# Optimization experiments

Measured on AMD Instinct MI355X. Metric: run time of the kernel, lower is better.

## Reference

```python
import jax, jax.numpy as jnp
import numpy as np

B, T, V, D, L, FFM = 2, 2048, 50257, 1024, 8, 2


def setup_inputs() -> dict:
    key = jax.random.key(0)
    ks = jax.random.split(key, 10)
    s = 0.02
    return {
        "input_ids": jax.random.randint(ks[0], (B, T), 0, V),
        "embed": jax.random.normal(ks[1], (V, D), jnp.float32) * s,
        "norm1_w": jnp.ones((L, D), jnp.float32),
        "norm2_w": jnp.ones((L, D), jnp.float32),
        "a_diag": jax.random.uniform(ks[2], (L, D), jnp.float32, 0.5, 0.99),
        "W_in": jax.random.normal(ks[3], (L, D, D), jnp.float32) * s,
        "b_in": jnp.zeros((L, D), jnp.float32),
        "W_out": jax.random.normal(ks[4], (L, D, D), jnp.float32) * s,
        "ff_w1": jax.random.normal(ks[5], (L, D, FFM * D), jnp.float32) * s,
        "ff_b1": jnp.zeros((L, FFM * D), jnp.float32),
        "ff_w2": jax.random.normal(ks[6], (L, FFM * D, D), jnp.float32) * s,
        "ff_b2": jnp.zeros((L, D), jnp.float32),
        "final_norm_w": jnp.ones((D,), jnp.float32),
        "lm_head_w": jax.random.normal(ks[7], (V, D), jnp.float32) * s,
    }


def rmsnorm(x, w, eps=1e-6):
    return x * jax.lax.rsqrt(jnp.mean(x * x, axis=-1, keepdims=True) + eps) * w


def chaos_core(x, a, Win, bin_, Wout):
    pre = jnp.einsum('btd,de->bte', x, Win) + bin_  # precompute input drive (parallel)

    def step(s, p):
        s = jnp.tanh(a * s + p)
        return s, s

    s0 = jnp.zeros((x.shape[0], x.shape[-1]), x.dtype)
    _, hs = jax.lax.scan(step, s0, jnp.swapaxes(pre, 0, 1))  # (T, B, D)
    hs = jnp.swapaxes(hs, 0, 1)  # (B, T, D)
    return jnp.einsum('btd,de->bte', hs, Wout)


def reference(input_ids, embed, norm1_w, norm2_w, a_diag, W_in, b_in, W_out,
              ff_w1, ff_b1, ff_w2, ff_b2, final_norm_w, lm_head_w):
    x = embed[input_ids]  # (B, T, D)
    for i in range(L):
        # input_norm -> core -> residual
        x = x + chaos_core(rmsnorm(x, norm1_w[i]), a_diag[i], W_in[i], b_in[i], W_out[i])
        # ff_norm -> FeedForward (Linear -> SiLU -> Linear) -> residual
        h = rmsnorm(x, norm2_w[i])
        h = jax.nn.silu(jnp.einsum('btd,df->btf', h, ff_w1[i]) + ff_b1[i])
        x = x + jnp.einsum('btf,fd->btd', h, ff_w2[i]) + ff_b2[i]
    x = rmsnorm(x, final_norm_w)
    return jnp.einsum('btd,vd->btv', x, lm_head_w)  # logits (B, T, V)
```

## Files before the change

### kernel.cpp

```cpp
#include <hip/hip_runtime.h>

typedef unsigned short u16;
typedef __bf16 bf16x8 __attribute__((ext_vector_type(8)));
typedef float f32x4 __attribute__((ext_vector_type(4)));
typedef unsigned short u16x4 __attribute__((ext_vector_type(4)));

__device__ __forceinline__ u16 f2bf(float f) {
  union { float f; unsigned int u; } v; v.f = f;
  return (u16)((v.u + 0x7FFFu + ((v.u >> 16) & 1u)) >> 16);
}

__device__ __forceinline__ void gload16(const void* g, void* l) {
  __builtin_amdgcn_global_load_lds(
      (const __attribute__((address_space(1))) unsigned int*)g,
      (__attribute__((address_space(3))) unsigned int*)l, 16, 0, 0);
}

__global__ __launch_bounds__(256) void prep_all(
    const float* __restrict__ Win, const float* __restrict__ Wout,
    const float* __restrict__ ffw1, const float* __restrict__ ffw2,
    u16* __restrict__ WinT, u16* __restrict__ WoutT,
    u16* __restrict__ f1T, u16* __restrict__ f2T,
    const float* __restrict__ lmw, u16* __restrict__ lmpad,
    const int* __restrict__ ids, const float* __restrict__ embedw,
    float* __restrict__ x) {
  __shared__ float tile[32][33];
  const int bid = blockIdx.x;
  const int tid = threadIdx.x;

  if (bid >= 49152 + 50432) {
    const int row = bid - (49152 + 50432);
    *(float4*)(x + (size_t)row * 1024 + tid * 4) =
        *(const float4*)(embedw + (size_t)ids[row] * 1024 + tid * 4);
    return;
  }
  if (bid >= 49152) {
    const int row = bid - 49152;
    u16x4 o = {0, 0, 0, 0};
    if (row < 50257) {
      float4 v = *(const float4*)(lmw + (size_t)row * 1024 + tid * 4);
      o.x = f2bf(v.x); o.y = f2bf(v.y); o.z = f2bf(v.z); o.w = f2bf(v.w);
    }
    *(u16x4*)(lmpad + (size_t)row * 1024 + tid * 4) = o;
    return;
  }

  const int tk = bid;
  const float* src; u16* dst;
  int R, C, tr, tc;
  if (tk < 8192) {
    const int l = tk >> 10, rem = tk & 1023;
    R = 1024; C = 1024; tr = rem >> 5; tc = rem & 31;
    src = Win + (size_t)l * 1048576; dst = WinT + (size_t)l * 1048576;
  } else if (tk < 16384) {
    const int q = tk - 8192, l = q >> 10, rem = q & 1023;
    R = 1024; C = 1024; tr = rem >> 5; tc = rem & 31;
    src = Wout + (size_t)l * 1048576; dst = WoutT + (size_t)l * 1048576;
  } else if (tk < 32768) {
    const int q = tk - 16384, l = q >> 11, rem = q & 2047;
    R = 1024; C = 2048; tr = rem >> 6; tc = rem & 63;
    src = ffw1 + (size_t)l * 2097152; dst = f1T + (size_t)l * 2097152;
  } else {
    const int q = tk - 32768, l = q >> 11, rem = q & 2047;
    R = 2048; C = 1024; tr = rem >> 5; tc = rem & 31;
    src = ffw2 + (size_t)l * 2097152; dst = f2T + (size_t)l * 2097152;
  }
  const int tx = tid & 31, ty = tid >> 5;
  const int c0 = tc * 32, r0 = tr * 32;
#pragma unroll
  for (int k = 0; k < 32; k += 8)
    tile[ty + k][tx] = src[(size_t)(r0 + ty + k) * C + (c0 + tx)];
  __syncthreads();
#pragma unroll
  for (int k = 0; k < 32; k += 8)
    dst[(size_t)(c0 + ty + k) * R + (r0 + tx)] = f2bf(tile[tx][ty + k]);
}

__global__ void rmsnorm_kernel(const float* __restrict__ x, const float* __restrict__ w,
                               u16* __restrict__ out) {
  const int row = blockIdx.x, tid = threadIdx.x;
  const float* xr = x + (size_t)row * 1024;
  float4 v = *(const float4*)(xr + tid * 4);
  float ss = v.x * v.x + v.y * v.y + v.z * v.z + v.w * v.w;
#pragma unroll
  for (int off = 32; off; off >>= 1) ss += __shfl_xor(ss, off);
  __shared__ float red[4];
  if ((tid & 63) == 0) red[tid >> 6] = ss;
  __syncthreads();
  const float tot = red[0] + red[1] + red[2] + red[3];
  const float r = rsqrtf(tot * (1.0f / 1024.0f) + 1e-6f);
  float4 wv = *(const float4*)(w + tid * 4);
  u16x4 o;
  o.x = f2bf(v.x * r * wv.x); o.y = f2bf(v.y * r * wv.y);
  o.z = f2bf(v.z * r * wv.z); o.w = f2bf(v.w * r * wv.w);
  *(u16x4*)(out + (size_t)row * 1024 + tid * 4) = o;
}

__device__ __forceinline__ void sload(const float* __restrict__ p, int tb,
                                      float A2b, float (&buf)[8]) {
#pragma unroll
  for (int j = 0; j < 8; j++)
    buf[j] = fmaf(p[(size_t)(tb + j) * 1024], 2.8853900817779268f, A2b);
}

__device__ __forceinline__ void scomp(float (&buf)[8], float m2A2, float& r,
                                      u16* __restrict__ o, int tb) {
#pragma unroll
  for (int j = 0; j < 8; j++) {
    float z = fmaf(m2A2, r, buf[j]);
    float e = __builtin_amdgcn_exp2f(z);
    r = __builtin_amdgcn_rcpf(1.0f + e);
    o[(size_t)(tb + j) * 1024] = f2bf(fmaf(-2.0f, r, 1.0f));
  }
}

__global__ __launch_bounds__(256) void scan_kernel(const float* __restrict__ pre,
                                                   const float* __restrict__ a_diag,
                                                   const float* __restrict__ b_in,
                                                   u16* __restrict__ hs) {
  const int T = 2048;
  const int idx = blockIdx.x * 256 + threadIdx.x;
  const int b = idx >> 10, d = idx & 1023;
  const float* p = pre + (size_t)b * T * 1024 + d;
  u16* o = hs + (size_t)b * T * 1024 + d;
  const float A2 = a_diag[d] * 2.8853900817779268f;
  const float A2b = fmaf(2.8853900817779268f, b_in[d], A2);
  const float m2A2 = -2.0f * A2;
  float r = 0.5f;
  float b0[8], b1[8], b2[8], b3[8];
  sload(p, 0, A2b, b0); sload(p, 8, A2b, b1);
  sload(p, 16, A2b, b2); sload(p, 24, A2b, b3);
  for (int t0 = 0; t0 < T; t0 += 32) {
    scomp(b0, m2A2, r, o, t0);
    if (t0 + 32 < T) sload(p, t0 + 32, A2b, b0);
    scomp(b1, m2A2, r, o, t0 + 8);
    if (t0 + 32 < T) sload(p, t0 + 40, A2b, b1);
    scomp(b2, m2A2, r, o, t0 + 16);
    if (t0 + 32 < T) sload(p, t0 + 48, A2b, b2);
    scomp(b3, m2A2, r, o, t0 + 24);
    if (t0 + 32 < T) sload(p, t0 + 56, A2b, b3);
  }
}

template <int EPI>
__global__ __launch_bounds__(256) void gemmL(
    const u16* __restrict__ A, int lda, const u16* __restrict__ Bw, int ldb,
    const float* __restrict__ bias, float* Cf, u16* __restrict__ Cb,
    int ldc, int K) {
  __shared__ char lds[49152];
  const int tid = threadIdx.x;
  const int lane = tid & 63;
  const int wc = tid >> 6;
  const int tm = blockIdx.y * 64, tn = blockIdx.x * 128;
  const int lr = lane & 15;
  const int sb0 = ((lane >> 4) ^ (lane & 7)) << 4;

  const int srow = tid >> 3;
  const int sxs = ((tid & 7) ^ (srow & 7)) << 4;
  const char* pA = (const char*)A + (size_t)(tm + srow) * lda * 2 + sxs;
  const char* pB = (const char*)Bw + (size_t)(tn + srow) * ldb * 2 + sxs;
  const size_t a32 = (size_t)lda * 64;
  const size_t b32 = (size_t)ldb * 64;

#define STGL(kt, bufo)                                \
  {                                                   \
    char* d = lds + (bufo) + tid * 16;                \
    const size_t kb = (size_t)(kt) << 7;              \
    gload16(pA + kb, d);                              \
    gload16(pA + a32 + kb, d + 4096);                 \
    gload16(pB + kb, d + 8192);                       \
    gload16(pB + b32 + kb, d + 12288);                \
    gload16(pB + 2 * b32 + kb, d + 16384);            \
    gload16(pB + 3 * b32 + kb, d + 20480);            \
  }

  f32x4 acc[4][2] = {};
  const int nkt = K >> 6;

  STGL(0, 0);
  int cur = 0;
  for (int kt = 0; kt < nkt; ++kt) {
    if (kt + 1 < nkt) {
      STGL(kt + 1, (cur ^ 1) * 24576);
      asm volatile("s_waitcnt vmcnt(6)" ::: "memory");
    } else {
      asm volatile("s_waitcnt vmcnt(0)" ::: "memory");
    }
    __builtin_amdgcn_s_barrier();
    const char* base = lds + cur * 24576;
    bf16x8 aF[4][2], bF[2][2];
#pragma unroll
    for (int m = 0; m < 4; m++)
#pragma unroll
      for (int ks = 0; ks < 2; ks++)
        aF[m][ks] =
            *(const bf16x8*)(base + (m * 16 + lr) * 128 + (sb0 ^ (ks << 6)));
#pragma unroll
    for (int n = 0; n < 2; n++)
#pragma unroll
      for (int ks = 0; ks < 2; ks++)
        bF[n][ks] = *(const bf16x8*)(base + 8192 +
                                     (wc * 32 + n * 16 + lr) * 128 +
                                     (sb0 ^ (ks << 6)));
#pragma unroll
    for (int ks = 0; ks < 2; ks++)
#pragma unroll
      for (int m = 0; m < 4; m++)
#pragma unroll
        for (int n = 0; n < 2; n++)
          acc[m][n] = __builtin_amdgcn_mfma_f32_16x16x32_bf16(
              aF[m][ks], bF[n][ks], acc[m][n], 0, 0, 0);
    __builtin_amdgcn_s_barrier();
    cur ^= 1;
  }
#undef STGL

  const int crow = tm + ((lane >> 4) << 2);
  const int ccol = tn + wc * 32 + lr;
#pragma unroll
  for (int m = 0; m < 4; m++) {
#pragma unroll
    for (int n = 0; n < 2; n++) {
      const int cg = ccol + n * 16;
      float bb = 0.0f;
      if (EPI == 2 || EPI == 3) bb = bias[cg];
#pragma unroll
      for (int j = 0; j < 4; j++) {
        const size_t off = (size_t)(crow + m * 16 + j) * ldc + cg;
        const float v = acc[m][n][j] + bb;
        if (EPI == 0) {
          Cf[off] = v;
        } else if (EPI == 1) {
          Cf[off] += v;
        } else if (EPI == 2) {
          const float sg = __builtin_amdgcn_rcpf(
              1.0f + __builtin_amdgcn_exp2f(-1.4426950408889634f * v));
          Cb[off] = f2bf(v * sg);
        } else {
          Cf[off] += v;
        }
      }
    }
  }
}

__global__ __launch_bounds__(512, 2) void gemm_lm8(
    const u16* __restrict__ A, const u16* __restrict__ Bw,
    float* __restrict__ C, int Nreal) {
  __shared__ char lds[131072];
  const int tid = threadIdx.x;
  const int lane = tid & 63;
  const int wid = tid >> 6;
  const int wr = wid >> 2;
  const int wc = wid & 3;
  const int bid = blockIdx.x;
  const int tm = (((bid & 7) << 1) + ((bid >> 3) & 1)) << 8;
  const int tn = (bid >> 4) << 8;

  const int srow = tid >> 3;
  const int sxor = ((tid & 7) ^ (srow & 7)) << 4;
  const char* pAs = (const char*)A + ((size_t)(tm + srow) << 11) + sxor;
  const char* pBs = (const char*)Bw + ((size_t)(tn + srow) << 11) + sxor;

#define STG(p, h, kt, ro)                                      \
  {                                                            \
    char* d = lds + (ro) + tid * 16;                           \
    const char* s = (p) + ((size_t)(h) << 18) + ((kt) << 7);   \
    gload16(s, d);                                             \
    gload16(s + (64ull << 11), d + 8192);                      \
  }

  const int lr = lane & 15;
  const int sb0 = (((lane >> 4) ^ (lane & 7)) << 4);
  const int sb[2] = {sb0, sb0 ^ 64};
  const int aB = wr * 16384 + lr * 128;
  const int bB = 32768 + (wc >> 1) * 16384 + ((wc & 1) * 64 + lr) * 128;

  bf16x8 aR[4][2], bR[2][2][2];
  f32x4 acc[8][4] = {};

#define LDA_Q(bufo, mq)                                                         \
  _Pragma("unroll") for (int m_ = 0; m_ < 4; m_++)                              \
  _Pragma("unroll") for (int k_ = 0; k_ < 2; k_++)                              \
      aR[m_][k_] = *(const bf16x8*)(lds + (bufo) + aB + (mq)*8192 + m_*2048 + sb[k_]);

#define LDB_Q(bufo, nq)                                                         \
  _Pragma("unroll") for (int n_ = 0; n_ < 2; n_++)                              \
  _Pragma("unroll") for (int k_ = 0; k_ < 2; k_++)                              \
      bR[nq][n_][k_] = *(const bf16x8*)(lds + (bufo) + bB + (nq)*4096 + n_*2048 + sb[k_]);

#define MFMA_Q(mq, nq)                                                          \
  __builtin_amdgcn_s_setprio(1);                                                \
  _Pragma("unroll") for (int m_ = 0; m_ < 4; m_++)                              \
  _Pragma("unroll") for (int n_ = 0; n_ < 2; n_++)                              \
  _Pragma("unroll") for (int k_ = 0; k_ < 2; k_++)                              \
      acc[(mq)*4 + m_][(nq)*2 + n_] = __builtin_amdgcn_mfma_f32_16x16x32_bf16(  \
          aR[m_][k_], bR[nq][n_][k_], acc[(mq)*4 + m_][(nq)*2 + n_], 0, 0, 0);  \
  __builtin_amdgcn_s_setprio(0);

#define BAR() __builtin_amdgcn_s_barrier()
#define LGKM0() asm volatile("s_waitcnt lgkmcnt(0)" ::: "memory")

  STG(pAs, 0, 0, 0);
  STG(pAs, 1, 0, 16384);
  STG(pBs, 0, 0, 32768);
  STG(pBs, 1, 0, 49152);
  STG(pBs, 0, 1, 65536 + 32768);
  STG(pBs, 1, 1, 65536 + 49152);
  asm volatile("s_waitcnt vmcnt(4)" ::: "memory");
  BAR();

  for (int it = 0; it < 8; ++it) {
    const int t1 = 2 * it + 1, t2 = 2 * it + 2, t3 = 2 * it + 3;
    const bool st = (it < 7);
    LDA_Q(0, 0); LDB_Q(0, 0);
    STG(pAs, 0, t1, 65536);
    BAR(); LGKM0(); MFMA_Q(0, 0); BAR();
    LDB_Q(0, 1);
    STG(pAs, 1, t1, 65536 + 16384);
    BAR(); LGKM0(); MFMA_Q(0, 1); BAR();
    LDA_Q(0, 1);
    if (st) STG(pBs, 0, t2, 32768);
    BAR(); LGKM0(); MFMA_Q(1, 0); BAR();
    if (st) STG(pBs, 1, t2, 49152);
    BAR(); LGKM0(); MFMA_Q(1, 1);
    if (st) { asm volatile("s_waitcnt vmcnt(4)" ::: "memory"); }
    else    { asm volatile("s_waitcnt vmcnt(0)" ::: "memory"); }
    BAR();
    LDA_Q(65536, 0); LDB_Q(65536, 0);
    if (st) STG(pAs, 0, t2, 0);
    BAR(); LGKM0(); MFMA_Q(0, 0); BAR();
    LDB_Q(65536, 1);
    if (st) STG(pAs, 1, t2, 16384);
    BAR(); LGKM0(); MFMA_Q(0, 1); BAR();
    LDA_Q(65536, 1);
    if (st) STG(pBs, 0, t3, 65536 + 32768);
    BAR(); LGKM0(); MFMA_Q(1, 0); BAR();
    if (st) STG(pBs, 1, t3, 65536 + 49152);
    BAR(); LGKM0(); MFMA_Q(1, 1);
    if (st) { asm volatile("s_waitcnt vmcnt(4)" ::: "memory"); }
    else    { asm volatile("s_waitcnt vmcnt(0)" ::: "memory"); }
    BAR();
  }
#undef STG
#undef LDA_Q
#undef LDB_Q
#undef MFMA_Q
#undef BAR
#undef LGKM0

  const int crow = tm + wr * 128 + ((lane >> 4) << 2);
  const int ccol = tn + wc * 64 + lr;
#pragma unroll
  for (int M_ = 0; M_ < 8; M_++) {
    const int r = crow + (M_ >> 2) * 64 + (M_ & 3) * 16;
#pragma unroll
    for (int N_ = 0; N_ < 4; N_++) {
      const int cg = ccol + (N_ >> 1) * 32 + (N_ & 1) * 16;
      if (cg < Nreal) {
#pragma unroll
        for (int j = 0; j < 4; j++)
          C[(size_t)(r + j) * Nreal + cg] = acc[M_][N_][j];
      }
    }
  }
}

extern "C" void kernel_launch(void* const* d_in, const int* in_sizes, int n_in,
                              void* d_out, int out_size, void* d_ws, size_t ws_size,
                              hipStream_t stream) {
  const int D = 1024, V = 50257, L = 8;
  const int M = 4096;
  const int Vpad = 50432;
  const size_t MD = (size_t)M * D;

  const int* ids = (const int*)d_in[0];
  const float* embedw = (const float*)d_in[1];
  const float* norm1_w = (const float*)d_in[2];
  const float* norm2_w = (const float*)d_in[3];
  const float* a_diag = (const float*)d_in[4];
  const float* W_in = (const float*)d_in[5];
  const float* b_in = (const float*)d_in[6];
  const float* W_out = (const float*)d_in[7];
  const float* ff_w1 = (const float*)d_in[8];
  const float* ff_b1 = (const float*)d_in[9];
  const float* ff_w2 = (const float*)d_in[10];
  const float* ff_b2 = (const float*)d_in[11];
  const float* final_norm_w = (const float*)d_in[12];
  const float* lm_head_w = (const float*)d_in[13];

  char* w = (char*)d_ws;
  float* x = (float*)w;   w += MD * 4;
  u16* h = (u16*)w;       w += MD * 2;
  float* pre = (float*)w; w += MD * 4;
  u16* hs = (u16*)w;      w += MD * 2;
  u16* hff = (u16*)w;     w += MD * 2 * 2;
  u16* WinT = (u16*)w;    w += (size_t)L * D * D * 2;
  u16* WoutT = (u16*)w;   w += (size_t)L * D * D * 2;
  u16* ffw1T = (u16*)w;   w += (size_t)L * 2 * D * D * 2;
  u16* ffw2T = (u16*)w;   w += (size_t)L * 2 * D * D * 2;
  u16* lmpad = (u16*)w;   w += (size_t)Vpad * D * 2;

  prep_all<<<49152 + Vpad + M, 256, 0, stream>>>(
      W_in, W_out, ff_w1, ff_w2, WinT, WoutT, ffw1T, ffw2T,
      lm_head_w, lmpad, ids, embedw, x);

  for (int l = 0; l < L; l++) {
    rmsnorm_kernel<<<M, 256, 0, stream>>>(x, norm1_w + (size_t)l * D, h);
    gemmL<0><<<dim3(8, 64), 256, 0, stream>>>(
        h, D, WinT + (size_t)l * D * D, D, nullptr, pre, nullptr, D, D);
    scan_kernel<<<8, 256, 0, stream>>>(pre, a_diag + (size_t)l * D,
                                       b_in + (size_t)l * D, hs);
    gemmL<1><<<dim3(8, 64), 256, 0, stream>>>(
        hs, D, WoutT + (size_t)l * D * D, D, nullptr, x, nullptr, D, D);
    rmsnorm_kernel<<<M, 256, 0, stream>>>(x, norm2_w + (size_t)l * D, h);
    gemmL<2><<<dim3(16, 64), 256, 0, stream>>>(
        h, D, ffw1T + (size_t)l * 2 * D * D, D, ff_b1 + (size_t)l * 2 * D,
        nullptr, hff, 2 * D, D);
    gemmL<3><<<dim3(8, 64), 256, 0, stream>>>(
        hff, 2 * D, ffw2T + (size_t)l * 2 * D * D, 2 * D,
        ff_b2 + (size_t)l * D, x, nullptr, D, 2 * D);
  }

  rmsnorm_kernel<<<M, 256, 0, stream>>>(x, final_norm_w, h);
  gemm_lm8<<<dim3(8 * 394), 512, 0, stream>>>(h, lmpad, (float*)d_out, V);
}
```

Baseline: 2.703 ms.

## Replace 256x256 eight-wave LM-head GEMM with simpler 128x128 double-buffered kernel

The LM-head GEMM moves from a 256x256 tile computed by 8 waves, with a hand-interleaved quarter-phase schedule over 128KB of LDS, to a 128x128 tile computed by 4 waves. The new kernel uses a plain double-buffered K loop: prefetch the next K tile, wait, barrier, then run all MFMAs. It uses 64KB of LDS and launches four times as many blocks, which raises occupancy and shrinks the partial tile at the vocabulary edge. In exchange, each tile reuses its operands less, so global and LDS traffic per FLOP goes up, and the finer-grained overlap of loads with MFMAs is lost.

```diff
diff --git a/kernel.cpp b/kernel.cpp
--- a/kernel.cpp
+++ b/kernel.cpp
@@ -244,123 +244,92 @@
   }
 }
 
-__global__ __launch_bounds__(512, 2) void gemm_lm8(
+__global__ __launch_bounds__(256) void gemm_lm128(
     const u16* __restrict__ A, const u16* __restrict__ Bw,
     float* __restrict__ C, int Nreal) {
-  __shared__ char lds[131072];
+  __shared__ char lds[65536];
   const int tid = threadIdx.x;
   const int lane = tid & 63;
   const int wid = tid >> 6;
-  const int wr = wid >> 2;
-  const int wc = wid & 3;
+  const int wm = wid >> 1, wn = wid & 1;
   const int bid = blockIdx.x;
-  const int tm = (((bid & 7) << 1) + ((bid >> 3) & 1)) << 8;
-  const int tn = (bid >> 4) << 8;
+  const int tm = (((bid & 7) << 2) + ((bid >> 3) & 3)) << 7;
+  const int tn = (bid >> 5) << 7;
+
+  const int lr = lane & 15;
+  const int sb0 = ((lane >> 4) ^ (lane & 7)) << 4;
+  const int sb[2] = {sb0, sb0 ^ 64};
 
   const int srow = tid >> 3;
-  const int sxor = ((tid & 7) ^ (srow & 7)) << 4;
-  const char* pAs = (const char*)A + ((size_t)(tm + srow) << 11) + sxor;
-  const char* pBs = (const char*)Bw + ((size_t)(tn + srow) << 11) + sxor;
-
-#define STG(p, h, kt, ro)                                      \
-  {                                                            \
-    char* d = lds + (ro) + tid * 16;                           \
-    const char* s = (p) + ((size_t)(h) << 18) + ((kt) << 7);   \
-    gload16(s, d);                                             \
-    gload16(s + (64ull << 11), d + 8192);                      \
-  }
-
-  const int lr = lane & 15;
-  const int sb0 = (((lane >> 4) ^ (lane & 7)) << 4);
-  const int sb[2] = {sb0, sb0 ^ 64};
-  const int aB = wr * 16384 + lr * 128;
-  const int bB = 32768 + (wc >> 1) * 16384 + ((wc & 1) * 64 + lr) * 128;
-
-  bf16x8 aR[4][2], bR[2][2][2];
-  f32x4 acc[8][4] = {};
-
-#define LDA_Q(bufo, mq)                                                         \
-  _Pragma("unroll") for (int m_ = 0; m_ < 4; m_++)                              \
-  _Pragma("unroll") for (int k_ = 0; k_ < 2; k_++)                              \
-      aR[m_][k_] = *(const bf16x8*)(lds + (bufo) + aB + (mq)*8192 + m_*2048 + sb[k_]);
-
-#define LDB_Q(bufo, nq)                                                         \
-  _Pragma("unroll") for (int n_ = 0; n_ < 2; n_++)                              \
-  _Pragma("unroll") for (int k_ = 0; k_ < 2; k_++)                              \
-      bR[nq][n_][k_] = *(const bf16x8*)(lds + (bufo) + bB + (nq)*4096 + n_*2048 + sb[k_]);
-
-#define MFMA_Q(mq, nq)                                                          \
-  __builtin_amdgcn_s_setprio(1);                                                \
-  _Pragma("unroll") for (int m_ = 0; m_ < 4; m_++)                              \
-  _Pragma("unroll") for (int n_ = 0; n_ < 2; n_++)                              \
-  _Pragma("unroll") for (int k_ = 0; k_ < 2; k_++)                              \
-      acc[(mq)*4 + m_][(nq)*2 + n_] = __builtin_amdgcn_mfma_f32_16x16x32_bf16(  \
-          aR[m_][k_], bR[nq][n_][k_], acc[(mq)*4 + m_][(nq)*2 + n_], 0, 0, 0);  \
-  __builtin_amdgcn_s_setprio(0);
-
-#define BAR() __builtin_amdgcn_s_barrier()
-#define LGKM0() asm volatile("s_waitcnt lgkmcnt(0)" ::: "memory")
-
-  STG(pAs, 0, 0, 0);
-  STG(pAs, 1, 0, 16384);
-  STG(pBs, 0, 0, 32768);
-  STG(pBs, 1, 0, 49152);
-  STG(pBs, 0, 1, 65536 + 32768);
-  STG(pBs, 1, 1, 65536 + 49152);
-  asm volatile("s_waitcnt vmcnt(4)" ::: "memory");
-  BAR();
-
-  for (int it = 0; it < 8; ++it) {
-    const int t1 = 2 * it + 1, t2 = 2 * it + 2, t3 = 2 * it + 3;
-    const bool st = (it < 7);
-    LDA_Q(0, 0); LDB_Q(0, 0);
-    STG(pAs, 0, t1, 65536);
-    BAR(); LGKM0(); MFMA_Q(0, 0); BAR();
-    LDB_Q(0, 1);
-    STG(pAs, 1, t1, 65536 + 16384);
-    BAR(); LGKM0(); MFMA_Q(0, 1); BAR();
-    LDA_Q(0, 1);
-    if (st) STG(pBs, 0, t2, 32768);
-    BAR(); LGKM0(); MFMA_Q(1, 0); BAR();
-    if (st) STG(pBs, 1, t2, 49152);
-    BAR(); LGKM0(); MFMA_Q(1, 1);
-    if (st) { asm volatile("s_waitcnt vmcnt(4)" ::: "memory"); }
-    else    { asm volatile("s_waitcnt vmcnt(0)" ::: "memory"); }
-    BAR();
-    LDA_Q(65536, 0); LDB_Q(65536, 0);
-    if (st) STG(pAs, 0, t2, 0);
-    BAR(); LGKM0(); MFMA_Q(0, 0); BAR();
-    LDB_Q(65536, 1);
-    if (st) STG(pAs, 1, t2, 16384);
-    BAR(); LGKM0(); MFMA_Q(0, 1); BAR();
-    LDA_Q(65536, 1);
-    if (st) STG(pBs, 0, t3, 65536 + 32768);
-    BAR(); LGKM0(); MFMA_Q(1, 0); BAR();
-    if (st) STG(pBs, 1, t3, 65536 + 49152);
-    BAR(); LGKM0(); MFMA_Q(1, 1);
-    if (st) { asm volatile("s_waitcnt vmcnt(4)" ::: "memory"); }
-    else    { asm volatile("s_waitcnt vmcnt(0)" ::: "memory"); }
-    BAR();
-  }
-#undef STG
-#undef LDA_Q
-#undef LDB_Q
-#undef MFMA_Q
-#undef BAR
-#undef LGKM0
-
-  const int crow = tm + wr * 128 + ((lane >> 4) << 2);
-  const int ccol = tn + wc * 64 + lr;
-#pragma unroll
-  for (int M_ = 0; M_ < 8; M_++) {
-    const int r = crow + (M_ >> 2) * 64 + (M_ & 3) * 16;
-#pragma unroll
-    for (int N_ = 0; N_ < 4; N_++) {
-      const int cg = ccol + (N_ >> 1) * 32 + (N_ & 1) * 16;
+  const int sxs = ((tid & 7) ^ (srow & 7)) << 4;
+  const char* pA = (const char*)A + ((size_t)(tm + srow) << 11) + sxs;
+  const char* pB = (const char*)Bw + ((size_t)(tn + srow) << 11) + sxs;
+  const size_t p32 = (size_t)32 << 11;
+
+#define STG128(kt, bufo)                               \
+  {                                                    \
+    char* d = lds + (bufo) + tid * 16;                 \
+    const size_t kb = (size_t)(kt) << 7;               \
+    gload16(pA + kb, d);                               \
+    gload16(pA + p32 + kb, d + 4096);                  \
+    gload16(pA + 2 * p32 + kb, d + 8192);              \
+    gload16(pA + 3 * p32 + kb, d + 12288);             \
+    gload16(pB + kb, d + 16384);                       \
+    gload16(pB + p32 + kb, d + 20480);                 \
+    gload16(pB + 2 * p32 + kb, d + 24576);             \
+    gload16(pB + 3 * p32 + kb, d + 28672);             \
+  }
+
+  const int aB0 = (wm * 64 + lr) * 128;
+  const int bB0 = 16384 + (wn * 64 + lr) * 128;
+
+  f32x4 acc[4][4] = {};
+
+  STG128(0, 0);
+  int cur = 0;
+  for (int kt = 0; kt < 16; ++kt) {
+    if (kt + 1 < 16) {
+      STG128(kt + 1, (cur ^ 1) * 32768);
+      asm volatile("s_waitcnt vmcnt(8)" ::: "memory");
+    } else {
+      asm volatile("s_waitcnt vmcnt(0)" ::: "memory");
+    }
+    __builtin_amdgcn_s_barrier();
+    const char* base = lds + cur * 32768;
+    bf16x8 aF[4][2], bF[4][2];
+#pragma unroll
+    for (int m = 0; m < 4; m++)
+#pragma unroll
+      for (int ks = 0; ks < 2; ks++) {
+        aF[m][ks] = *(const bf16x8*)(base + aB0 + m * 2048 + sb[ks]);
+        bF[m][ks] = *(const bf16x8*)(base + bB0 + m * 2048 + sb[ks]);
+      }
+    __builtin_amdgcn_s_setprio(1);
+#pragma unroll
+    for (int ks = 0; ks < 2; ks++)
+#pragma unroll
+      for (int m = 0; m < 4; m++)
+#pragma unroll
+        for (int n = 0; n < 4; n++)
+          acc[m][n] = __builtin_amdgcn_mfma_f32_16x16x32_bf16(
+              aF[m][ks], bF[n][ks], acc[m][n], 0, 0, 0);
+    __builtin_amdgcn_s_setprio(0);
+    __builtin_amdgcn_s_barrier();
+    cur ^= 1;
+  }
+#undef STG128
+
+  const int crow = tm + wm * 64 + ((lane >> 4) << 2);
+  const int ccol = tn + wn * 64 + lr;
+#pragma unroll
+  for (int m = 0; m < 4; m++) {
+#pragma unroll
+    for (int n = 0; n < 4; n++) {
+      const int cg = ccol + n * 16;
       if (cg < Nreal) {
 #pragma unroll
         for (int j = 0; j < 4; j++)
-          C[(size_t)(r + j) * Nreal + cg] = acc[M_][N_][j];
+          C[(size_t)(crow + m * 16 + j) * Nreal + cg] = acc[m][n][j];
       }
     }
   }
@@ -423,5 +392,5 @@
   }
 
   rmsnorm_kernel<<<M, 256, 0, stream>>>(x, final_norm_w, h);
-  gemm_lm8<<<dim3(8 * 394), 512, 0, stream>>>(h, lmpad, (float*)d_out, V);
-}
+  gemm_lm128<<<dim3(32 * 394), 256, 0, stream>>>(h, lmpad, (float*)d_out, V);
+}
```

New measurement: 2.779 ms. 2.8% more time.
